# Optimization experiments

Measured on AMD Instinct MI355X. Metric: run time of the kernel, lower is better.

The kernel has to match this reference:

```python
import jax, jax.numpy as jnp
import numpy as np

NX = 1024
N_HEAD = 16
B = 2
N = 2048


def setup_inputs() -> dict:
    key = jax.random.key(0)
    k1, k2, k3 = jax.random.split(key, 3)
    x = jax.random.normal(k1, (B, N, NX), dtype=jnp.float32)
    # masked_fill mask: True where attention is NOT allowed (above diagonal)
    mask_self_attention = ~jnp.tril(jnp.ones((N, N), dtype=bool))[None, None]
    c_attn_w = jax.random.normal(k2, (NX, 3 * NX), dtype=jnp.float32) * 0.02
    c_attn_b = jnp.zeros((3 * NX,), dtype=jnp.float32)
    c_proj_w = jax.random.normal(k3, (NX, NX), dtype=jnp.float32) * 0.02
    c_proj_b = jnp.zeros((NX,), dtype=jnp.float32)
    return {
        'x': x,
        'c_attn_w': c_attn_w,
        'c_attn_b': c_attn_b,
        'c_proj_w': c_proj_w,
        'c_proj_b': c_proj_b,
        'mask_self_attention': mask_self_attention,
    }


def reference(x, c_attn_w, c_attn_b, c_proj_w, c_proj_b, mask_self_attention):
    hd = NX // N_HEAD  # head dim = 64
    qkv = x @ c_attn_w + c_attn_b                      # [B,N,3*NX]
    q, k, v = jnp.split(qkv, 3, axis=-1)
    # split heads -> [B,H,N,hd]
    q = q.reshape(B, N, N_HEAD, hd).transpose(0, 2, 1, 3)
    v = v.reshape(B, N, N_HEAD, hd).transpose(0, 2, 1, 3)
    k_t = k.reshape(B, N, N_HEAD, hd).transpose(0, 2, 3, 1)  # [B,H,hd,N]
    present = jnp.stack((k_t.transpose(0, 1, 3, 2), v))      # [2,B,H,N,hd]
    w = jnp.einsum('bhqd,bhdk->bhqk', q, k_t)
    w = w / jnp.sqrt(jnp.float32(hd))  # scale=True
    w = jnp.where(mask_self_attention, jnp.float32(-10000.0), w)
    w = jax.nn.softmax(w, axis=-1)
    a = jnp.einsum('bhqk,bhkd->bhqd', w, v)            # [B,H,N,hd]
    a = a.transpose(0, 2, 1, 3).reshape(B, N, NX)      # merge heads
    a = a @ c_proj_w + c_proj_b
    return (a, present)
```

## Files before the change

### kernel.cpp

```cpp
#include <hip/hip_runtime.h>
#include <cstddef>
#include <cstdint>

#define NX_ 1024
#define NH_ 16
#define HD_ 64
#define B_  2
#define N_  2048
#define M_  (B_ * N_)

typedef __attribute__((ext_vector_type(8))) short bf16x8;
typedef __attribute__((ext_vector_type(4))) float f32x4;

__device__ __forceinline__ unsigned short f2bf(float f) {
    union { float f; unsigned u; } v; v.f = f;
    return (unsigned short)((v.u + 0x7FFFu + ((v.u >> 16) & 1u)) >> 16);
}
__device__ __forceinline__ unsigned pk2bf(float a, float b) {
    return (unsigned)f2bf(a) | ((unsigned)f2bf(b) << 16);
}
__device__ __forceinline__ unsigned pkrnd(float a, float b) {
    union { float f; unsigned u; } ua, ub; ua.f = a; ub.f = b;
    return __builtin_amdgcn_perm(ub.u + 0x8000u, ua.u + 0x8000u, 0x07060302u);
}
__device__ __forceinline__ float exp2_hw(float x) {
    float r;
    asm("v_exp_f32 %0, %1" : "=v"(r) : "v"(x));
    return r;
}

__device__ __forceinline__ void gload_lds16(const void* g, void* l) {
    __builtin_amdgcn_global_load_lds(
        (const __attribute__((address_space(1))) unsigned int*)g,
        (__attribute__((address_space(3))) unsigned int*)l, 16, 0, 0);
}

__global__ __launch_bounds__(256)
void pre_pass(const float* __restrict__ x, unsigned short* __restrict__ xb,
              const float* __restrict__ wqkv, unsigned short* __restrict__ wqkv_t,
              const float* __restrict__ wpr, unsigned short* __restrict__ wproj_t)
{
    const int bid = blockIdx.x, t = threadIdx.x;
    if (bid < 2048) {
        const size_t i = ((size_t)bid * 256 + t) * 8;
        const float4 a = *(const float4*)(x + i);
        const float4 b = *(const float4*)(x + i + 4);
        uint4 o;
        o.x = pk2bf(a.x, a.y); o.y = pk2bf(a.z, a.w);
        o.z = pk2bf(b.x, b.y); o.w = pk2bf(b.z, b.w);
        *(uint4*)(xb + i) = o;
        return;
    }
    __shared__ unsigned short tile[32][40];
    const float* W; unsigned short* Wt; int ncols, n0, k0;
    if (bid < 2048 + 3072) {
        const int b2 = bid - 2048;
        W = wqkv; Wt = wqkv_t; ncols = 3072; n0 = (b2 % 96) * 32; k0 = (b2 / 96) * 32;
    } else {
        const int b3 = bid - 5120;
        W = wpr; Wt = wproj_t; ncols = 1024; n0 = (b3 & 31) * 32; k0 = (b3 >> 5) * 32;
    }
    const int r = t >> 3, c4 = (t & 7) * 4;
    const float4 v = *(const float4*)(W + (size_t)(k0 + r) * ncols + n0 + c4);
    tile[r][c4 + 0] = f2bf(v.x); tile[r][c4 + 1] = f2bf(v.y);
    tile[r][c4 + 2] = f2bf(v.z); tile[r][c4 + 3] = f2bf(v.w);
    __syncthreads();
    uint2 o;
    o.x = (unsigned)tile[c4 + 0][r] | ((unsigned)tile[c4 + 1][r] << 16);
    o.y = (unsigned)tile[c4 + 2][r] | ((unsigned)tile[c4 + 3][r] << 16);
    *(uint2*)(Wt + (size_t)(n0 + r) * 1024 + k0 + c4) = o;
}

template<int NOUT, int MODE, int GX>
__global__ __launch_bounds__(256, 3)
void gemm_mfma(const unsigned short* __restrict__ Ab, const unsigned short* __restrict__ Wt,
               const float* __restrict__ bias,
               float* __restrict__ o_pk, float* __restrict__ o_pv,
               unsigned short* __restrict__ o_q, unsigned short* __restrict__ o_k,
               unsigned short* __restrict__ o_vt, float* __restrict__ o_f)
{
    __shared__ __align__(16) unsigned short As[2][128 * 32];
    __shared__ __align__(16) unsigned short Bs[2][128 * 32];
    const int t = threadIdx.x, l = t & 63;
    const int g = l >> 4, q15 = l & 15;
    const int w = t >> 6, wm = w >> 1, wn = w & 1;

    const int nwg = GX * 32;
    const int swz = ((int)blockIdx.x & 7) * (nwg / 8) + ((int)blockIdx.x >> 3);
    const int m0 = (swz / GX) * 128, j0 = (swz % GX) * 128;

    f32x4 acc[4][4];
#pragma unroll
    for (int i = 0; i < 4; i++)
#pragma unroll
        for (int j = 0; j < 4; j++) { acc[i][j][0]=0.f; acc[i][j][1]=0.f; acc[i][j][2]=0.f; acc[i][j][3]=0.f; }

    const int srow[2] = { (w * 2 + 0) * 16 + (l >> 2), (w * 2 + 1) * 16 + (l >> 2) };
    const int kct0 = ((l & 3) ^ (srow[0] & 3) ^ ((srow[0] >> 2) & 3)) & 3;
    const int kct1 = ((l & 3) ^ (srow[1] & 3) ^ ((srow[1] >> 2) & 3)) & 3;

#define STAGE(BUF, K0)                                                          \
    do {                                                                        \
        gload_lds16(Ab + (size_t)(m0 + srow[0]) * 1024 + (K0) + kct0 * 8,       \
                    &As[BUF][(w * 2 + 0) * 64 * 8]);                            \
        gload_lds16(Ab + (size_t)(m0 + srow[1]) * 1024 + (K0) + kct1 * 8,       \
                    &As[BUF][(w * 2 + 1) * 64 * 8]);                            \
        gload_lds16(Wt + (size_t)(j0 + srow[0]) * 1024 + (K0) + kct0 * 8,       \
                    &Bs[BUF][(w * 2 + 0) * 64 * 8]);                            \
        gload_lds16(Wt + (size_t)(j0 + srow[1]) * 1024 + (K0) + kct1 * 8,       \
                    &Bs[BUF][(w * 2 + 1) * 64 * 8]);                            \
    } while (0)

    STAGE(0, 0);
    __syncthreads();

    for (int k0 = 0; k0 < 1024; k0 += 32) {
        const int buf = (k0 >> 5) & 1;
        if (k0 + 32 < 1024) STAGE(buf ^ 1, k0 + 32);

        bf16x8 af[4], bf[4];
#pragma unroll
        for (int mt = 0; mt < 4; mt++) {
            const int m = wm * 64 + mt * 16 + q15;
            af[mt] = *(const bf16x8*)&As[buf][m * 32 + ((g ^ (m & 3) ^ ((m >> 2) & 3)) & 3) * 8];
        }
#pragma unroll
        for (int nt = 0; nt < 4; nt++) {
            const int n = wn * 64 + nt * 16 + q15;
            bf[nt] = *(const bf16x8*)&Bs[buf][n * 32 + ((g ^ (n & 3) ^ ((n >> 2) & 3)) & 3) * 8];
        }
#pragma unroll
        for (int mt = 0; mt < 4; mt++)
#pragma unroll
            for (int nt = 0; nt < 4; nt++)
                acc[mt][nt] = __builtin_amdgcn_mfma_f32_16x16x32_bf16(af[mt], bf[nt], acc[mt][nt], 0, 0, 0);

        __syncthreads();
    }

#pragma unroll
    for (int nt = 0; nt < 4; nt++) {
        const int ncol = wn * 64 + nt * 16 + q15;
        const int jc = j0 + ncol;
        const float bz = bias[jc];
        const int sec = jc >> 10, jl = jc & 1023, hh = jl >> 6, dd = jl & 63;
#pragma unroll
        for (int mt = 0; mt < 4; mt++) {
#pragma unroll
            for (int r = 0; r < 4; r++) {
                const int m = m0 + wm * 64 + mt * 16 + g * 4 + r;
                const float val = acc[mt][nt][r] + bz;
                if (MODE == 1) {
                    o_f[(size_t)m * NOUT + jc] = val;
                } else {
                    const int bb = m >> 11, nn = m & 2047;
                    const int bhh = bb * NH_ + hh;
                    const size_t idx = ((size_t)bhh * N_ + nn) * HD_ + dd;
                    if (sec == 0)      o_q[idx] = f2bf(val * 0.18033688f);
                    else if (sec == 1) { o_pk[idx] = val; o_k[idx] = f2bf(val); }
                    else               { o_pv[idx] = val;
                                         o_vt[((size_t)bhh * HD_ + dd) * N_ + nn] = f2bf(val); }
                }
            }
        }
    }
#undef STAGE
}

__global__ __launch_bounds__(512, 2)
void attn_mfma(const unsigned short* __restrict__ q_bf,
               const unsigned short* __restrict__ k_bf,
               const unsigned short* __restrict__ v_t,
               unsigned short* __restrict__ a_pre)
{
    __shared__ __align__(16) unsigned short Ks[2][64 * 64];
    __shared__ __align__(16) unsigned short Vt[2][64 * 64];
    __shared__ __align__(16) unsigned short Ps[128 * 64];

    const int t = threadIdx.x, l = t & 63, w = t >> 6;
    const int g = l >> 4, q15 = l & 15;

    const int bid = (int)blockIdx.x;
    const int x = bid & 7, r = bid >> 3;
    const int bh = x * 4 + (r & 3);
    const int j = r >> 2;
    const int qt = (j < 8) ? (15 - j) : (j - 8);
    const int b = bh >> 4, h = bh & 15;

    const unsigned short* kb  = k_bf + (size_t)bh * N_ * HD_;
    const unsigned short* vtb = v_t  + (size_t)bh * HD_ * N_;

    const int qrow = w * 16 + q15;
    const int qg = qt * 128 + qrow;
    const unsigned short* qp = q_bf + ((size_t)bh * N_ + qg) * HD_ + g * 8;
    const bf16x8 qf0 = *(const bf16x8*)(qp);
    const bf16x8 qf1 = *(const bf16x8*)(qp + 32);

    const int sr = t >> 3, s8 = t & 7;
    uint4 stgK, stgV;

#define ISSUE(KT)                                                               \
    do {                                                                        \
        stgK = *(const uint4*)(kb + ((size_t)((KT) * 64 + sr)) * HD_ + s8 * 8); \
        stgV = *(const uint4*)(vtb + (size_t)sr * N_ + (KT) * 64 + s8 * 8);     \
    } while (0)

#define COMMIT(BUF)                                                             \
    do {                                                                        \
        *(uint4*)&Ks[BUF][sr * 64 + ((s8 ^ (sr & 7)) & 7) * 8] = stgK;          \
        *(uint4*)&Vt[BUF][sr * 64 + ((s8 ^ (sr & 7)) & 7) * 8] = stgV;          \
    } while (0)

    ISSUE(0); COMMIT(0);
    __syncthreads();

    float l_i = 0.f;
    f32x4 oacc[4];
#pragma unroll
    for (int i = 0; i < 4; i++) { oacc[i][0]=0.f; oacc[i][1]=0.f; oacc[i][2]=0.f; oacc[i][3]=0.f; }

    int cur = 0;
    char* const prow = (char*)Ps + qrow * 128;
    const int psw = (qrow & 7) << 4;
    const int ktmax = 2 * qt + 1;

    for (int kt = 0; kt <= ktmax; kt++) {
        const bool more = (kt < ktmax);
        if (more) ISSUE(kt + 1);

        f32x4 sacc[4];
#pragma unroll
        for (int i = 0; i < 4; i++) { sacc[i][0]=0.f; sacc[i][1]=0.f; sacc[i][2]=0.f; sacc[i][3]=0.f; }
        __builtin_amdgcn_s_setprio(1);
#pragma unroll
        for (int kt4 = 0; kt4 < 4; kt4++) {
            const int row = kt4 * 16 + q15;
            const bf16x8 kf0 = *(const bf16x8*)&Ks[cur][row * 64 + ((g ^ (row & 7)) & 7) * 8];
            sacc[kt4] = __builtin_amdgcn_mfma_f32_16x16x32_bf16(kf0, qf0, sacc[kt4], 0, 0, 0);
            const bf16x8 kf1 = *(const bf16x8*)&Ks[cur][row * 64 + (((g + 4) ^ (row & 7)) & 7) * 8];
            sacc[kt4] = __builtin_amdgcn_mfma_f32_16x16x32_bf16(kf1, qf1, sacc[kt4], 0, 0, 0);
        }
        __builtin_amdgcn_s_setprio(0);

        float pe[16];
        if (kt >= 2 * qt) {
#pragma unroll
            for (int kt4 = 0; kt4 < 4; kt4++)
#pragma unroll
                for (int rr = 0; rr < 4; rr++) {
                    const int kcg = kt * 64 + kt4 * 16 + g * 4 + rr;
                    const float s = (kcg > qg) ? -1.0e30f : sacc[kt4][rr];
                    pe[kt4 * 4 + rr] = exp2_hw(s);
                }
        } else {
#pragma unroll
            for (int kt4 = 0; kt4 < 4; kt4++)
#pragma unroll
                for (int rr = 0; rr < 4; rr++) pe[kt4 * 4 + rr] = exp2_hw(sacc[kt4][rr]);
        }
        {
            float s8v[8];
#pragma unroll
            for (int i = 0; i < 8; i++) s8v[i] = pe[2 * i] + pe[2 * i + 1];
            const float s0 = (s8v[0] + s8v[1]) + (s8v[2] + s8v[3]);
            const float s1 = (s8v[4] + s8v[5]) + (s8v[6] + s8v[7]);
            l_i += s0 + s1;
        }
#pragma unroll
        for (int kt4 = 0; kt4 < 4; kt4++) {
            uint2 w2;
            w2.x = pkrnd(pe[kt4 * 4 + 0], pe[kt4 * 4 + 1]);
            w2.y = pkrnd(pe[kt4 * 4 + 2], pe[kt4 * 4 + 3]);
            *(uint2*)(prow + ((kt4 * 32 + g * 8) ^ psw)) = w2;
        }

        {
            const bf16x8 pf0 = *(const bf16x8*)(prow + ((g * 16) ^ psw));
            const bf16x8 pf1 = *(const bf16x8*)(prow + (((g + 4) * 16) ^ psw));
            __builtin_amdgcn_s_setprio(1);
#pragma unroll
            for (int dt = 0; dt < 4; dt++) {
                const int vrow = dt * 16 + q15;
                const bf16x8 vf = *(const bf16x8*)&Vt[cur][vrow * 64 + ((g ^ (vrow & 7)) & 7) * 8];
                oacc[dt] = __builtin_amdgcn_mfma_f32_16x16x32_bf16(vf, pf0, oacc[dt], 0, 0, 0);
            }
#pragma unroll
            for (int dt = 0; dt < 4; dt++) {
                const int vrow = dt * 16 + q15;
                const bf16x8 vf = *(const bf16x8*)&Vt[cur][vrow * 64 + (((g + 4) ^ (vrow & 7)) & 7) * 8];
                oacc[dt] = __builtin_amdgcn_mfma_f32_16x16x32_bf16(vf, pf1, oacc[dt], 0, 0, 0);
            }
            __builtin_amdgcn_s_setprio(0);
        }

        if (more) COMMIT(cur ^ 1);
        __syncthreads();
        cur ^= 1;
    }

    float lt = l_i;
    lt += __shfl_xor(lt, 16);
    lt += __shfl_xor(lt, 32);
    const float inv = 1.0f / lt;

    unsigned short* ap2 = a_pre + ((size_t)(b * N_ + qg)) * NX_ + h * 64;
#pragma unroll
    for (int dt = 0; dt < 4; dt++) {
#pragma unroll
        for (int j2 = 0; j2 < 2; j2++) {
            const int d = dt * 16 + g * 4 + j2 * 2;
            *(unsigned*)(ap2 + d) = pkrnd(oacc[dt][j2 * 2] * inv, oacc[dt][j2 * 2 + 1] * inv);
        }
    }
#undef ISSUE
#undef COMMIT
}

extern "C" void kernel_launch(void* const* d_in, const int* in_sizes, int n_in,
                              void* d_out, int out_size, void* d_ws, size_t ws_size,
                              hipStream_t stream)
{
    (void)in_sizes; (void)n_in; (void)out_size; (void)ws_size;
    const float* x    = (const float*)d_in[0];
    const float* wqkv = (const float*)d_in[1];
    const float* bqkv = (const float*)d_in[2];
    const float* wpr  = (const float*)d_in[3];
    const float* bpr  = (const float*)d_in[4];

    float* out   = (float*)d_out;
    float* a_out = out;
    float* pk    = out + (size_t)M_ * NX_;
    float* pv    = pk + (size_t)B_ * NH_ * N_ * HD_;

    const size_t SEG = (size_t)M_ * NX_;
    unsigned short* xb      = (unsigned short*)d_ws;
    unsigned short* q_bf    = xb + SEG;
    unsigned short* k_bf    = q_bf + SEG;
    unsigned short* v_t     = k_bf + SEG;
    unsigned short* wqkv_t  = v_t + SEG;
    unsigned short* wproj_t = wqkv_t + (size_t)3 * NX_ * NX_;
    unsigned short* a_pre   = xb;

    pre_pass<<<2048 + 3072 + 1024, 256, 0, stream>>>(x, xb, wqkv, wqkv_t, wpr, wproj_t);

    gemm_mfma<3 * NX_, 0, 24><<<768, 256, 0, stream>>>(
        xb, wqkv_t, bqkv, pk, pv, q_bf, k_bf, v_t, nullptr);
    attn_mfma<<<512, 512, 0, stream>>>(q_bf, k_bf, v_t, a_pre);
    gemm_mfma<NX_, 1, 8><<<256, 256, 0, stream>>>(
        a_pre, wproj_t, bpr, nullptr, nullptr, nullptr, nullptr, nullptr, a_out);
}
```

Baseline: 198.8 us.

## Triple-buffer GEMM LDS pipeline with single barrier and XCD-aware tile mapping

Changes the projection GEMM mainloop from double to triple buffering. Loads are issued two k-steps ahead, with an explicit vmcnt wait and one barrier per iteration instead of two syncs. MFMA blocks are wrapped in s_setprio, and the block-to-tile mapping now groups column tiles per XCD to improve L2 reuse of weights. Shared memory grows by half, which may reduce occupancy under the 3-blocks-per-SM launch bound.

```diff
diff --git a/kernel.cpp b/kernel.cpp
--- a/kernel.cpp
+++ b/kernel.cpp
@@ -79,21 +79,22 @@
                unsigned short* __restrict__ o_q, unsigned short* __restrict__ o_k,
                unsigned short* __restrict__ o_vt, float* __restrict__ o_f)
 {
-    __shared__ __align__(16) unsigned short As[2][128 * 32];
-    __shared__ __align__(16) unsigned short Bs[2][128 * 32];
+    __shared__ __align__(16) unsigned short As[3][128 * 32];
+    __shared__ __align__(16) unsigned short Bs[3][128 * 32];
     const int t = threadIdx.x, l = t & 63;
     const int g = l >> 4, q15 = l & 15;
     const int w = t >> 6, wm = w >> 1, wn = w & 1;
 
-    const int nwg = GX * 32;
-    const int swz = ((int)blockIdx.x & 7) * (nwg / 8) + ((int)blockIdx.x >> 3);
-    const int m0 = (swz / GX) * 128, j0 = (swz % GX) * 128;
+    const int xcd = (int)blockIdx.x & 7, i = (int)blockIdx.x >> 3;
+    constexpr int CPX = GX / 8;
+    const int j0 = (xcd * CPX + i % CPX) * 128;
+    const int m0 = (i / CPX) * 128;
 
     f32x4 acc[4][4];
 #pragma unroll
-    for (int i = 0; i < 4; i++)
-#pragma unroll
-        for (int j = 0; j < 4; j++) { acc[i][j][0]=0.f; acc[i][j][1]=0.f; acc[i][j][2]=0.f; acc[i][j][3]=0.f; }
+    for (int ii = 0; ii < 4; ii++)
+#pragma unroll
+        for (int jj = 0; jj < 4; jj++) { acc[ii][jj][0]=0.f; acc[ii][jj][1]=0.f; acc[ii][jj][2]=0.f; acc[ii][jj][3]=0.f; }
 
     const int srow[2] = { (w * 2 + 0) * 16 + (l >> 2), (w * 2 + 1) * 16 + (l >> 2) };
     const int kct0 = ((l & 3) ^ (srow[0] & 3) ^ ((srow[0] >> 2) & 3)) & 3;
@@ -111,32 +112,45 @@
                     &Bs[BUF][(w * 2 + 1) * 64 * 8]);                            \
     } while (0)
 
+#define COMPUTE(BUF)                                                            \
+    do {                                                                        \
+        bf16x8 af[4], bfv[4];                                                   \
+        _Pragma("unroll")                                                       \
+        for (int mt = 0; mt < 4; mt++) {                                        \
+            const int m = wm * 64 + mt * 16 + q15;                              \
+            af[mt] = *(const bf16x8*)&As[BUF][m * 32 + ((g ^ (m & 3) ^ ((m >> 2) & 3)) & 3) * 8]; \
+        }                                                                       \
+        _Pragma("unroll")                                                       \
+        for (int nt = 0; nt < 4; nt++) {                                        \
+            const int n = wn * 64 + nt * 16 + q15;                              \
+            bfv[nt] = *(const bf16x8*)&Bs[BUF][n * 32 + ((g ^ (n & 3) ^ ((n >> 2) & 3)) & 3) * 8]; \
+        }                                                                       \
+        __builtin_amdgcn_s_setprio(1);                                          \
+        _Pragma("unroll")                                                       \
+        for (int mt = 0; mt < 4; mt++)                                          \
+            _Pragma("unroll")                                                   \
+            for (int nt = 0; nt < 4; nt++)                                      \
+                acc[mt][nt] = __builtin_amdgcn_mfma_f32_16x16x32_bf16(af[mt], bfv[nt], acc[mt][nt], 0, 0, 0); \
+        __builtin_amdgcn_s_setprio(0);                                          \
+    } while (0)
+
+    constexpr int NK = 1024 / 32;
     STAGE(0, 0);
-    __syncthreads();
-
-    for (int k0 = 0; k0 < 1024; k0 += 32) {
-        const int buf = (k0 >> 5) & 1;
-        if (k0 + 32 < 1024) STAGE(buf ^ 1, k0 + 32);
-
-        bf16x8 af[4], bf[4];
-#pragma unroll
-        for (int mt = 0; mt < 4; mt++) {
-            const int m = wm * 64 + mt * 16 + q15;
-            af[mt] = *(const bf16x8*)&As[buf][m * 32 + ((g ^ (m & 3) ^ ((m >> 2) & 3)) & 3) * 8];
-        }
-#pragma unroll
-        for (int nt = 0; nt < 4; nt++) {
-            const int n = wn * 64 + nt * 16 + q15;
-            bf[nt] = *(const bf16x8*)&Bs[buf][n * 32 + ((g ^ (n & 3) ^ ((n >> 2) & 3)) & 3) * 8];
-        }
-#pragma unroll
-        for (int mt = 0; mt < 4; mt++)
-#pragma unroll
-            for (int nt = 0; nt < 4; nt++)
-                acc[mt][nt] = __builtin_amdgcn_mfma_f32_16x16x32_bf16(af[mt], bf[nt], acc[mt][nt], 0, 0, 0);
-
-        __syncthreads();
-    }
+    STAGE(1, 32);
+
+    int b0 = 0;
+    for (int k0 = 0; k0 < NK - 1; ++k0) {
+        asm volatile("s_waitcnt vmcnt(4)" ::: "memory");
+        __builtin_amdgcn_sched_barrier(0);
+        __builtin_amdgcn_s_barrier();
+        if (k0 + 2 < NK) STAGE((b0 + 2 >= 3 ? b0 - 1 : b0 + 2), (k0 + 2) * 32);
+        COMPUTE(b0);
+        b0 = (b0 + 1 == 3) ? 0 : b0 + 1;
+    }
+    asm volatile("s_waitcnt vmcnt(0)" ::: "memory");
+    __builtin_amdgcn_sched_barrier(0);
+    __builtin_amdgcn_s_barrier();
+    COMPUTE(b0);
 
 #pragma unroll
     for (int nt = 0; nt < 4; nt++) {
@@ -165,6 +179,7 @@
         }
     }
 #undef STAGE
+#undef COMPUTE
 }
 
 __global__ __launch_bounds__(512, 2)
```

Result: slower. 212.2 us (+6.8%).

## Split-K output projection with atomics and transpose V inside attention LDS staging

Applied to the files above, without the earlier changes.

The output projection GEMM now splits K into two halves across 512 blocks, fills 256 CUs better than the previous 256-block launch, and accumulates partial results into a zeroed output with float atomicAdd (bias added only by the first split). The QKV GEMM now writes V in row-major bf16 instead of a strided transposed layout, and the attention kernel transposes V into LDS during staging with scalar 16-bit stores. This removes scattered global transposed writes, at the cost of an extra memset, atomic traffic, non-deterministic summation order, and slower element-wise LDS writes in attention.

```diff
diff --git a/kernel.cpp b/kernel.cpp
--- a/kernel.cpp
+++ b/kernel.cpp
@@ -77,7 +77,7 @@
                const float* __restrict__ bias,
                float* __restrict__ o_pk, float* __restrict__ o_pv,
                unsigned short* __restrict__ o_q, unsigned short* __restrict__ o_k,
-               unsigned short* __restrict__ o_vt, float* __restrict__ o_f)
+               unsigned short* __restrict__ o_vb, float* __restrict__ o_f)
 {
     __shared__ __align__(16) unsigned short As[2][128 * 32];
     __shared__ __align__(16) unsigned short Bs[2][128 * 32];
@@ -85,15 +85,25 @@
     const int g = l >> 4, q15 = l & 15;
     const int w = t >> 6, wm = w >> 1, wn = w & 1;
 
-    const int nwg = GX * 32;
-    const int swz = ((int)blockIdx.x & 7) * (nwg / 8) + ((int)blockIdx.x >> 3);
-    const int m0 = (swz / GX) * 128, j0 = (swz % GX) * 128;
+    int m0, j0, kofs, nks;
+    if (MODE == 2) {
+        const int ks = (int)blockIdx.x >> 8;
+        const int inner = (int)blockIdx.x & 255;
+        const int swz = (inner & 7) * 32 + (inner >> 3);
+        m0 = (swz >> 3) * 128; j0 = (swz & 7) * 128;
+        kofs = ks * 512; nks = 16;
+    } else {
+        constexpr int nwg = GX * 32;
+        const int swz = ((int)blockIdx.x & 7) * (nwg / 8) + ((int)blockIdx.x >> 3);
+        m0 = (swz / GX) * 128; j0 = (swz % GX) * 128;
+        kofs = 0; nks = 32;
+    }
 
     f32x4 acc[4][4];
 #pragma unroll
-    for (int i = 0; i < 4; i++)
-#pragma unroll
-        for (int j = 0; j < 4; j++) { acc[i][j][0]=0.f; acc[i][j][1]=0.f; acc[i][j][2]=0.f; acc[i][j][3]=0.f; }
+    for (int ii = 0; ii < 4; ii++)
+#pragma unroll
+        for (int jj = 0; jj < 4; jj++) { acc[ii][jj][0]=0.f; acc[ii][jj][1]=0.f; acc[ii][jj][2]=0.f; acc[ii][jj][3]=0.f; }
 
     const int srow[2] = { (w * 2 + 0) * 16 + (l >> 2), (w * 2 + 1) * 16 + (l >> 2) };
     const int kct0 = ((l & 3) ^ (srow[0] & 3) ^ ((srow[0] >> 2) & 3)) & 3;
@@ -111,14 +121,14 @@
                     &Bs[BUF][(w * 2 + 1) * 64 * 8]);                            \
     } while (0)
 
-    STAGE(0, 0);
+    STAGE(0, kofs);
     __syncthreads();
 
-    for (int k0 = 0; k0 < 1024; k0 += 32) {
-        const int buf = (k0 >> 5) & 1;
-        if (k0 + 32 < 1024) STAGE(buf ^ 1, k0 + 32);
-
-        bf16x8 af[4], bf[4];
+    for (int kk = 0; kk < nks; ++kk) {
+        const int buf = kk & 1;
+        if (kk + 1 < nks) STAGE(buf ^ 1, kofs + (kk + 1) * 32);
+
+        bf16x8 af[4], bfv[4];
 #pragma unroll
         for (int mt = 0; mt < 4; mt++) {
             const int m = wm * 64 + mt * 16 + q15;
@@ -127,13 +137,13 @@
 #pragma unroll
         for (int nt = 0; nt < 4; nt++) {
             const int n = wn * 64 + nt * 16 + q15;
-            bf[nt] = *(const bf16x8*)&Bs[buf][n * 32 + ((g ^ (n & 3) ^ ((n >> 2) & 3)) & 3) * 8];
+            bfv[nt] = *(const bf16x8*)&Bs[buf][n * 32 + ((g ^ (n & 3) ^ ((n >> 2) & 3)) & 3) * 8];
         }
 #pragma unroll
         for (int mt = 0; mt < 4; mt++)
 #pragma unroll
             for (int nt = 0; nt < 4; nt++)
-                acc[mt][nt] = __builtin_amdgcn_mfma_f32_16x16x32_bf16(af[mt], bf[nt], acc[mt][nt], 0, 0, 0);
+                acc[mt][nt] = __builtin_amdgcn_mfma_f32_16x16x32_bf16(af[mt], bfv[nt], acc[mt][nt], 0, 0, 0);
 
         __syncthreads();
     }
@@ -142,7 +152,7 @@
     for (int nt = 0; nt < 4; nt++) {
         const int ncol = wn * 64 + nt * 16 + q15;
         const int jc = j0 + ncol;
-        const float bz = bias[jc];
+        const float bz = (MODE == 2 && kofs != 0) ? 0.f : bias[jc];
         const int sec = jc >> 10, jl = jc & 1023, hh = jl >> 6, dd = jl & 63;
 #pragma unroll
         for (int mt = 0; mt < 4; mt++) {
@@ -150,16 +160,15 @@
             for (int r = 0; r < 4; r++) {
                 const int m = m0 + wm * 64 + mt * 16 + g * 4 + r;
                 const float val = acc[mt][nt][r] + bz;
-                if (MODE == 1) {
-                    o_f[(size_t)m * NOUT + jc] = val;
+                if (MODE == 2) {
+                    atomicAdd(&o_f[(size_t)m * NOUT + jc], val);
                 } else {
                     const int bb = m >> 11, nn = m & 2047;
                     const int bhh = bb * NH_ + hh;
                     const size_t idx = ((size_t)bhh * N_ + nn) * HD_ + dd;
                     if (sec == 0)      o_q[idx] = f2bf(val * 0.18033688f);
                     else if (sec == 1) { o_pk[idx] = val; o_k[idx] = f2bf(val); }
-                    else               { o_pv[idx] = val;
-                                         o_vt[((size_t)bhh * HD_ + dd) * N_ + nn] = f2bf(val); }
+                    else               { o_pv[idx] = val; o_vb[idx] = f2bf(val); }
                 }
             }
         }
@@ -170,7 +179,7 @@
 __global__ __launch_bounds__(512, 2)
 void attn_mfma(const unsigned short* __restrict__ q_bf,
                const unsigned short* __restrict__ k_bf,
-               const unsigned short* __restrict__ v_t,
+               const unsigned short* __restrict__ v_bf,
                unsigned short* __restrict__ a_pre)
 {
     __shared__ __align__(16) unsigned short Ks[2][64 * 64];
@@ -187,8 +196,8 @@
     const int qt = (j < 8) ? (15 - j) : (j - 8);
     const int b = bh >> 4, h = bh & 15;
 
-    const unsigned short* kb  = k_bf + (size_t)bh * N_ * HD_;
-    const unsigned short* vtb = v_t  + (size_t)bh * HD_ * N_;
+    const unsigned short* kb = k_bf + (size_t)bh * N_ * HD_;
+    const unsigned short* vb = v_bf + (size_t)bh * N_ * HD_;
 
     const int qrow = w * 16 + q15;
     const int qg = qt * 128 + qrow;
@@ -197,18 +206,26 @@
     const bf16x8 qf1 = *(const bf16x8*)(qp + 32);
 
     const int sr = t >> 3, s8 = t & 7;
+    const int vn = t & 63, vd0 = (t >> 6) * 8;
     uint4 stgK, stgV;
 
 #define ISSUE(KT)                                                               \
     do {                                                                        \
         stgK = *(const uint4*)(kb + ((size_t)((KT) * 64 + sr)) * HD_ + s8 * 8); \
-        stgV = *(const uint4*)(vtb + (size_t)sr * N_ + (KT) * 64 + s8 * 8);     \
+        stgV = *(const uint4*)(vb + ((size_t)((KT) * 64 + vn)) * HD_ + vd0);    \
     } while (0)
 
-#define COMMIT(BUF)                                                             \
-    do {                                                                        \
-        *(uint4*)&Ks[BUF][sr * 64 + ((s8 ^ (sr & 7)) & 7) * 8] = stgK;          \
-        *(uint4*)&Vt[BUF][sr * 64 + ((s8 ^ (sr & 7)) & 7) * 8] = stgV;          \
+#define COMMIT(BUF)                                                            \
+    do {                                                                       \
+        *(uint4*)&Ks[BUF][sr * 64 + ((s8 ^ (sr & 7)) & 7) * 8] = stgK;         \
+        const unsigned* vu = (const unsigned*)&stgV;                           \
+        _Pragma("unroll")                                                      \
+        for (int jj = 0; jj < 8; jj++) {                                       \
+            const unsigned short e =                                           \
+                (unsigned short)(vu[jj >> 1] >> ((jj & 1) * 16));              \
+            const int vd = vd0 + jj;                                           \
+            Vt[BUF][vd * 64 + ((((vn >> 3) ^ (vd & 7)) & 7) * 8 + (vn & 7))] = e; \
+        }                                                                      \
     } while (0)
 
     ISSUE(0); COMMIT(0);
@@ -336,16 +353,18 @@
     unsigned short* xb      = (unsigned short*)d_ws;
     unsigned short* q_bf    = xb + SEG;
     unsigned short* k_bf    = q_bf + SEG;
-    unsigned short* v_t     = k_bf + SEG;
-    unsigned short* wqkv_t  = v_t + SEG;
+    unsigned short* v_bf    = k_bf + SEG;
+    unsigned short* wqkv_t  = v_bf + SEG;
     unsigned short* wproj_t = wqkv_t + (size_t)3 * NX_ * NX_;
     unsigned short* a_pre   = xb;
 
+    hipMemsetAsync(a_out, 0, (size_t)M_ * NX_ * sizeof(float), stream);
+
     pre_pass<<<2048 + 3072 + 1024, 256, 0, stream>>>(x, xb, wqkv, wqkv_t, wpr, wproj_t);
 
     gemm_mfma<3 * NX_, 0, 24><<<768, 256, 0, stream>>>(
-        xb, wqkv_t, bqkv, pk, pv, q_bf, k_bf, v_t, nullptr);
-    attn_mfma<<<512, 512, 0, stream>>>(q_bf, k_bf, v_t, a_pre);
-    gemm_mfma<NX_, 1, 8><<<256, 256, 0, stream>>>(
+        xb, wqkv_t, bqkv, pk, pv, q_bf, k_bf, v_bf, nullptr);
+    attn_mfma<<<512, 512, 0, stream>>>(q_bf, k_bf, v_bf, a_pre);
+    gemm_mfma<NX_, 2, 8><<<512, 256, 0, stream>>>(
         a_pre, wproj_t, bpr, nullptr, nullptr, nullptr, nullptr, nullptr, a_out);
 }
```

Result: slower. 223.1 us (+12.2%).

## Use XCD-aware tile mapping and narrower N tile for projection GEMM

Applied to the files above, without the earlier changes.

Replaces the block-index swizzle with an XCD-aware mapping that gives each pair of XCDs a contiguous group of M panels and a half of the N panels, so blocks on the same XCD share A and B panels in L2. The output projection GEMM now uses 64-wide N tiles and 512 blocks instead of 256, so more blocks are available to fill the CUs. The trade-off is less reuse per block (lower arithmetic intensity) in exchange for better occupancy and cache locality.

```diff
diff --git a/kernel.cpp b/kernel.cpp
--- a/kernel.cpp
+++ b/kernel.cpp
@@ -71,76 +71,86 @@
     *(uint2*)(Wt + (size_t)(n0 + r) * 1024 + k0 + c4) = o;
 }
 
-template<int NOUT, int MODE, int GX>
-__global__ __launch_bounds__(256, 3)
+template<int NOUT, int MODE, int BN, int JPX, int OCC>
+__global__ __launch_bounds__(256, OCC)
 void gemm_mfma(const unsigned short* __restrict__ Ab, const unsigned short* __restrict__ Wt,
                const float* __restrict__ bias,
                float* __restrict__ o_pk, float* __restrict__ o_pv,
                unsigned short* __restrict__ o_q, unsigned short* __restrict__ o_k,
                unsigned short* __restrict__ o_vt, float* __restrict__ o_f)
 {
+    constexpr int NT = BN / 32;
     __shared__ __align__(16) unsigned short As[2][128 * 32];
-    __shared__ __align__(16) unsigned short Bs[2][128 * 32];
+    __shared__ __align__(16) unsigned short Bs[2][BN * 32];
     const int t = threadIdx.x, l = t & 63;
     const int g = l >> 4, q15 = l & 15;
     const int w = t >> 6, wm = w >> 1, wn = w & 1;
 
-    const int nwg = GX * 32;
-    const int swz = ((int)blockIdx.x & 7) * (nwg / 8) + ((int)blockIdx.x >> 3);
-    const int m0 = (swz / GX) * 128, j0 = (swz % GX) * 128;
-
-    f32x4 acc[4][4];
-#pragma unroll
-    for (int i = 0; i < 4; i++)
-#pragma unroll
-        for (int j = 0; j < 4; j++) { acc[i][j][0]=0.f; acc[i][j][1]=0.f; acc[i][j][2]=0.f; acc[i][j][3]=0.f; }
-
-    const int srow[2] = { (w * 2 + 0) * 16 + (l >> 2), (w * 2 + 1) * 16 + (l >> 2) };
-    const int kct0 = ((l & 3) ^ (srow[0] & 3) ^ ((srow[0] >> 2) & 3)) & 3;
-    const int kct1 = ((l & 3) ^ (srow[1] & 3) ^ ((srow[1] >> 2) & 3)) & 3;
+    const int xcd = (int)blockIdx.x & 7, i = (int)blockIdx.x >> 3;
+    const int mpanel = (xcd >> 1) * 8 + i / JPX;
+    const int jpanel = (xcd & 1) * JPX + i % JPX;
+    const int m0 = mpanel * 128, j0 = jpanel * BN;
+
+    f32x4 acc[4][NT];
+#pragma unroll
+    for (int ii = 0; ii < 4; ii++)
+#pragma unroll
+        for (int jj = 0; jj < NT; jj++) { acc[ii][jj][0]=0.f; acc[ii][jj][1]=0.f; acc[ii][jj][2]=0.f; acc[ii][jj][3]=0.f; }
+
+    const int srowA0 = (w * 2 + 0) * 16 + (l >> 2);
+    const int srowA1 = (w * 2 + 1) * 16 + (l >> 2);
+    const int kctA0 = ((l & 3) ^ (srowA0 & 3) ^ ((srowA0 >> 2) & 3)) & 3;
+    const int kctA1 = ((l & 3) ^ (srowA1 & 3) ^ ((srowA1 >> 2) & 3)) & 3;
+    const int srowB  = w * 16 + (l >> 2);
+    const int kctB  = ((l & 3) ^ (srowB & 3) ^ ((srowB >> 2) & 3)) & 3;
 
 #define STAGE(BUF, K0)                                                          \
     do {                                                                        \
-        gload_lds16(Ab + (size_t)(m0 + srow[0]) * 1024 + (K0) + kct0 * 8,       \
-                    &As[BUF][(w * 2 + 0) * 64 * 8]);                            \
-        gload_lds16(Ab + (size_t)(m0 + srow[1]) * 1024 + (K0) + kct1 * 8,       \
-                    &As[BUF][(w * 2 + 1) * 64 * 8]);                            \
-        gload_lds16(Wt + (size_t)(j0 + srow[0]) * 1024 + (K0) + kct0 * 8,       \
-                    &Bs[BUF][(w * 2 + 0) * 64 * 8]);                            \
-        gload_lds16(Wt + (size_t)(j0 + srow[1]) * 1024 + (K0) + kct1 * 8,       \
-                    &Bs[BUF][(w * 2 + 1) * 64 * 8]);                            \
+        gload_lds16(Ab + (size_t)(m0 + srowA0) * 1024 + (K0) + kctA0 * 8,       \
+                    &As[BUF][(w * 2 + 0) * 512]);                               \
+        gload_lds16(Ab + (size_t)(m0 + srowA1) * 1024 + (K0) + kctA1 * 8,       \
+                    &As[BUF][(w * 2 + 1) * 512]);                               \
+        if (BN == 128) {                                                        \
+            gload_lds16(Wt + (size_t)(j0 + srowA0) * 1024 + (K0) + kctA0 * 8,   \
+                        &Bs[BUF][(w * 2 + 0) * 512]);                           \
+            gload_lds16(Wt + (size_t)(j0 + srowA1) * 1024 + (K0) + kctA1 * 8,   \
+                        &Bs[BUF][(w * 2 + 1) * 512]);                           \
+        } else {                                                                \
+            gload_lds16(Wt + (size_t)(j0 + srowB) * 1024 + (K0) + kctB * 8,     \
+                        &Bs[BUF][w * 512]);                                     \
+        }                                                                       \
     } while (0)
 
     STAGE(0, 0);
     __syncthreads();
 
-    for (int k0 = 0; k0 < 1024; k0 += 32) {
-        const int buf = (k0 >> 5) & 1;
-        if (k0 + 32 < 1024) STAGE(buf ^ 1, k0 + 32);
-
-        bf16x8 af[4], bf[4];
+    for (int kk = 0; kk < 32; ++kk) {
+        const int buf = kk & 1;
+        if (kk + 1 < 32) STAGE(buf ^ 1, (kk + 1) * 32);
+
+        bf16x8 af[4], bfv[NT];
 #pragma unroll
         for (int mt = 0; mt < 4; mt++) {
             const int m = wm * 64 + mt * 16 + q15;
             af[mt] = *(const bf16x8*)&As[buf][m * 32 + ((g ^ (m & 3) ^ ((m >> 2) & 3)) & 3) * 8];
         }
 #pragma unroll
-        for (int nt = 0; nt < 4; nt++) {
-            const int n = wn * 64 + nt * 16 + q15;
-            bf[nt] = *(const bf16x8*)&Bs[buf][n * 32 + ((g ^ (n & 3) ^ ((n >> 2) & 3)) & 3) * 8];
+        for (int nt = 0; nt < NT; nt++) {
+            const int n = wn * (BN / 2) + nt * 16 + q15;
+            bfv[nt] = *(const bf16x8*)&Bs[buf][n * 32 + ((g ^ (n & 3) ^ ((n >> 2) & 3)) & 3) * 8];
         }
 #pragma unroll
         for (int mt = 0; mt < 4; mt++)
 #pragma unroll
-            for (int nt = 0; nt < 4; nt++)
-                acc[mt][nt] = __builtin_amdgcn_mfma_f32_16x16x32_bf16(af[mt], bf[nt], acc[mt][nt], 0, 0, 0);
+            for (int nt = 0; nt < NT; nt++)
+                acc[mt][nt] = __builtin_amdgcn_mfma_f32_16x16x32_bf16(af[mt], bfv[nt], acc[mt][nt], 0, 0, 0);
 
         __syncthreads();
     }
 
 #pragma unroll
-    for (int nt = 0; nt < 4; nt++) {
-        const int ncol = wn * 64 + nt * 16 + q15;
+    for (int nt = 0; nt < NT; nt++) {
+        const int ncol = wn * (BN / 2) + nt * 16 + q15;
         const int jc = j0 + ncol;
         const float bz = bias[jc];
         const int sec = jc >> 10, jl = jc & 1023, hh = jl >> 6, dd = jl & 63;
@@ -343,9 +353,9 @@
 
     pre_pass<<<2048 + 3072 + 1024, 256, 0, stream>>>(x, xb, wqkv, wqkv_t, wpr, wproj_t);
 
-    gemm_mfma<3 * NX_, 0, 24><<<768, 256, 0, stream>>>(
+    gemm_mfma<3 * NX_, 0, 128, 12, 3><<<768, 256, 0, stream>>>(
         xb, wqkv_t, bqkv, pk, pv, q_bf, k_bf, v_t, nullptr);
     attn_mfma<<<512, 512, 0, stream>>>(q_bf, k_bf, v_t, a_pre);
-    gemm_mfma<NX_, 1, 8><<<256, 256, 0, stream>>>(
+    gemm_mfma<NX_, 1, 64, 8, 2><<<512, 256, 0, stream>>>(
         a_pre, wproj_t, bpr, nullptr, nullptr, nullptr, nullptr, nullptr, a_out);
 }
```

Measured after the change: 202.8 us. +2.0%, slower.
